# Kernel optimization log

Hardware: AMD Instinct MI355X
Metric: run time of the kernel (lower is better)

The kernel has to match this reference:

```python
import jax, jax.numpy as jnp
import numpy as np

DIM, HID, BATCH = 64, 512, 8192


def setup_inputs() -> dict:
    key = jax.random.key(0)
    ks = jax.random.split(key, 6)
    s1 = 1.0 / np.sqrt(DIM + 1)
    s2 = 1.0 / np.sqrt(HID)
    return {
        "t": jax.random.uniform(ks[0], (1,), dtype=jnp.float32),
        "x": jax.random.normal(ks[1], (BATCH, DIM), dtype=jnp.float32),
        "W1": jax.random.normal(ks[2], (DIM + 1, HID), dtype=jnp.float32) * s1,
        "b1": jnp.zeros((HID,), jnp.float32),
        "W2": jax.random.normal(ks[3], (HID, HID), dtype=jnp.float32) * s2,
        "b2": jnp.zeros((HID,), jnp.float32),
        "W3": jax.random.normal(ks[4], (HID, DIM), dtype=jnp.float32) * s2,
        "b3": jnp.zeros((DIM,), jnp.float32),
    }


def _vf_single(ts, xs, W1, b1, W2, b2, W3, b3):
    # xs: [dim], ts: scalar. Time concatenated as extra input feature.
    h = jnp.concatenate([xs, ts[None]])          # [dim+1]
    h = jnp.tanh(h @ W1 + b1)                    # [hid]
    h = jnp.tanh(h @ W2 + b2)                    # [hid]
    return h @ W3 + b3                           # [dim]


def reference(t, x, W1, b1, W2, b2, W3, b3):
    ts = t[0]
    vf = lambda xs: _vf_single(ts, xs, W1, b1, W2, b2, W3, b3)
    v = jax.vmap(vf)(x)                                   # [B, dim]
    # Exact divergence: trace of per-sample Jacobian dv/dx.
    # (Replaces the torch per-dim autograd.grad loop with one batched jacfwd.)
    J = jax.vmap(jax.jacfwd(vf))(x)                       # [B, dim, dim]
    div = jnp.trace(J, axis1=-2, axis2=-1)                # [B]
    return (v, -div[:, None])
```

## Files before the change

### kernel.cpp

```cpp
#include <hip/hip_runtime.h>

#define DIM 64
#define HID 512
#define BATCH 8192
#define MB 32
#define NTHR 1024

typedef __attribute__((ext_vector_type(8))) short short8;
typedef __attribute__((ext_vector_type(4))) float f32x4;
typedef __attribute__((ext_vector_type(16))) float f32x16;
typedef float float4_ __attribute__((ext_vector_type(4)));
typedef unsigned long long ull;

#define Z16 {0.f,0.f,0.f,0.f,0.f,0.f,0.f,0.f,0.f,0.f,0.f,0.f,0.f,0.f,0.f,0.f}

union U8 { short8 s8; unsigned short u[8]; };
union U4 { ull v; unsigned short u[4]; };
union FB { unsigned u; float f; };

__device__ __forceinline__ unsigned short f2bf(float f) {
    union { float f; unsigned u; } v; v.f = f;
    return (unsigned short)((v.u + 0x7FFFu + ((v.u >> 16) & 1u)) >> 16);
}
__device__ __forceinline__ float bf2f(unsigned short b) {
    FB v; v.u = (unsigned)b << 16; return v.f;
}
__device__ __forceinline__ float tanh_fast(float x) {
    float e = __expf(2.f * x);
    return 1.f - __fdividef(2.f, e + 1.f);
}

__global__ __launch_bounds__(256) void prep(
        const float* __restrict__ t,  const float* __restrict__ W1,
        const float* __restrict__ b1, const float* __restrict__ W2,
        const float* __restrict__ W3,
        unsigned short* __restrict__ w2pk, unsigned short* __restrict__ ppk,
        unsigned short* __restrict__ w3pk, unsigned short* __restrict__ w1pk,
        float* __restrict__ c1) {
    __shared__ float w3sT[DIM * 33];
    __shared__ float w1s[DIM * DIM];
    int b = blockIdx.x;
    if (b >= 288) {
        int n = (b - 288) * 256 + threadIdx.x;
        c1[n] = fmaf(t[0], W1[DIM * HID + n], b1[n]);
        return;
    }
    int gid = b * 256 + threadIdx.x;
    int f = gid >> 6, l = gid & 63;
    if (f < 512) {
        int nt = f >> 5, ks = f & 31;
        int n = nt * 32 + (l & 31), k0 = ks * 16 + (l >> 5) * 8;
        unsigned short* o = w2pk + (size_t)(f * 64 + l) * 8;
#pragma unroll
        for (int e = 0; e < 8; ++e) o[e] = f2bf(W2[(size_t)(k0 + e) * HID + n]);
    } else if (f < 1024) {
        int ntb = (b * 4 - 512) >> 5;
        int jb  = (((b - 128) * 4) & 31) * 16;
        for (int idx = threadIdx.x; idx < 32 * DIM; idx += 256) {
            int dn = idx >> 6, i = idx & 63;
            w3sT[i * 33 + dn] = W3[(size_t)(ntb * 32 + dn) * DIM + i];
        }
        for (int idx = threadIdx.x; idx < DIM * DIM; idx += 256) {
            int i = idx >> 6, jj = idx & 63;
            w1s[i * DIM + jj] = W1[(size_t)i * HID + jb + jj];
        }
        __syncthreads();
        int fi = f - 512;
        int ks = fi & 31;
        int dn = l & 31, k0 = ks * 16 + (l >> 5) * 8;
        int n = ntb * 32 + dn;
        int jo = k0 - jb;
        float m[8] = {0.f,0.f,0.f,0.f,0.f,0.f,0.f,0.f};
#pragma unroll
        for (int i = 0; i < DIM; ++i) {
            float w3 = w3sT[i * 33 + dn];
            const float* wrow = &w1s[i * DIM + jo];
#pragma unroll
            for (int e = 0; e < 8; ++e) m[e] = fmaf(wrow[e], w3, m[e]);
        }
        unsigned short* o = ppk + (size_t)(fi * 64 + l) * 8;
#pragma unroll
        for (int e = 0; e < 8; ++e) o[e] = f2bf(W2[(size_t)(k0 + e) * HID + n] * m[e]);
    } else if (f < 1088) {
        int fi = f - 1024;
        int nt = fi >> 4, ks = fi & 15;
        int n = nt * 16 + (l & 15), k0 = ks * 32 + (l >> 4) * 8;
        unsigned short* o = w3pk + (size_t)(fi * 64 + l) * 8;
#pragma unroll
        for (int e = 0; e < 8; ++e) o[e] = f2bf(W3[(size_t)(k0 + e) * DIM + n]);
    } else {
        int fi = f - 1088;
        int nt = fi >> 1, ks = fi & 1;
        int n = nt * 16 + (l & 15), k0 = ks * 32 + (l >> 4) * 8;
        unsigned short* o = w1pk + (size_t)(fi * 64 + l) * 8;
#pragma unroll
        for (int e = 0; e < 8; ++e) o[e] = f2bf(W1[(size_t)(k0 + e) * HID + n]);
    }
}

__device__ __forceinline__ int act_addr(int sample, int colbyte) {
    return (sample * 1024 + colbyte) ^ ((sample & 15) << 4);
}

__global__ __launch_bounds__(NTHR)
__attribute__((amdgpu_waves_per_eu(4, 4)))
void fused_main(
        const float* __restrict__ x,  const float* __restrict__ c1,
        const float* __restrict__ b2, const float* __restrict__ b3,
        const unsigned short* __restrict__ w1pk, const unsigned short* __restrict__ w2pk,
        const unsigned short* __restrict__ ppk,  const unsigned short* __restrict__ w3pk,
        float* __restrict__ out) {
    __shared__ unsigned short h1s[MB * HID];
    __shared__ unsigned short d1s[MB * HID];
    __shared__ unsigned short h2s[MB * HID];
    __shared__ float wred[8][MB];
    char* h1b = (char*)h1s; char* d1b = (char*)d1s; char* h2b = (char*)h2s;

    const int tid = threadIdx.x, w = tid >> 6, l = tid & 63;
    const int lr = l & 15, g = l >> 4;
    const int bid = blockIdx.x;
    const int s0 = bid * MB;

    short8 xf[2][2];
#pragma unroll
    for (int nt = 0; nt < 2; ++nt)
#pragma unroll
        for (int ks = 0; ks < 2; ++ks) {
            const float* xp = x + (size_t)(s0 + nt * 16 + lr) * DIM + ks * 32 + g * 8;
            float4_ x0 = *(const float4_*)xp;
            float4_ x1 = *(const float4_*)(xp + 4);
            U8 u;
            u.u[0]=f2bf(x0.x); u.u[1]=f2bf(x0.y); u.u[2]=f2bf(x0.z); u.u[3]=f2bf(x0.w);
            u.u[4]=f2bf(x1.x); u.u[5]=f2bf(x1.y); u.u[6]=f2bf(x1.z); u.u[7]=f2bf(x1.w);
            xf[nt][ks] = u.s8;
        }
#pragma unroll
    for (int mi = 0; mi < 2; ++mi) {
        int mt = w * 2 + mi;
        short8 a0 = ((const short8*)w1pk)[(size_t)((mt * 2 + 0) * 64 + l)];
        short8 a1 = ((const short8*)w1pk)[(size_t)((mt * 2 + 1) * 64 + l)];
        float c1q[4];
#pragma unroll
        for (int r = 0; r < 4; ++r) c1q[r] = c1[mt * 16 + g * 4 + r];
#pragma unroll
        for (int nt = 0; nt < 2; ++nt) {
            f32x4 acc = {0.f, 0.f, 0.f, 0.f};
            acc = __builtin_amdgcn_mfma_f32_16x16x32_bf16(a0, xf[nt][0], acc, 0, 0, 0);
            acc = __builtin_amdgcn_mfma_f32_16x16x32_bf16(a1, xf[nt][1], acc, 0, 0, 0);
            int sample = nt * 16 + lr;
            U4 hu, du;
#pragma unroll
            for (int r = 0; r < 4; ++r) {
                float h = tanh_fast(acc[r] + c1q[r]);
                hu.u[r] = f2bf(h);
                du.u[r] = f2bf(fmaf(-h, h, 1.f));
            }
            int ab = act_addr(sample, (mt * 16 + g * 4) * 2);
            *(ull*)(h1b + ab) = hu.v;
            *(ull*)(d1b + ab) = du.v;
        }
    }
    __syncthreads();

    const int q = w & 7, role = w >> 3;
    const int q2 = (q + bid) & 7;
    const short8* Bf = (const short8*)(role ? ppk : w2pk);
    const char* Ab = role ? d1b : h1b;
    const short8* b0p = Bf + (size_t)((2 * q2 + 0) * 32) * 64 + l;
    const short8* b1p = Bf + (size_t)((2 * q2 + 1) * 32) * 64 + l;
    const int rot = (bid * 5) & 31;
    f32x16 a0 = Z16, a1 = Z16;
#pragma unroll 4
    for (int i = 0; i < 32; ++i) {
        int ks = (i + rot) & 31;
        int ab = act_addr(l & 31, ks * 32 + (l >> 5) * 16);
        short8 av  = *(const short8*)(Ab + ab);
        short8 b0v = b0p[ks * 64];
        short8 b1v = b1p[ks * 64];
        a0 = __builtin_amdgcn_mfma_f32_32x32x16_bf16(av, b0v, a0, 0, 0, 0);
        a1 = __builtin_amdgcn_mfma_f32_32x32x16_bf16(av, b1v, a1, 0, 0, 0);
    }

    if (role == 0) {
#pragma unroll
        for (int j = 0; j < 2; ++j) {
            int c = (2 * q2 + j) * 32 + (l & 31);
            float b2v = b2[c];
            f32x16 acc = j ? a1 : a0;
#pragma unroll
            for (int r = 0; r < 16; ++r) {
                int row = (r & 3) + 8 * (r >> 2) + 4 * (l >> 5);
                float h2 = tanh_fast(acc[r] + b2v);
                *(unsigned short*)(h2b + act_addr(row, c * 2)) = f2bf(h2);
            }
        }
    }
    __syncthreads();

    if (role == 1) {
        float divp[16];
#pragma unroll
        for (int r = 0; r < 16; ++r) divp[r] = 0.f;
#pragma unroll
        for (int j = 0; j < 2; ++j) {
            int c = (2 * q2 + j) * 32 + (l & 31);
            f32x16 acc = j ? a1 : a0;
#pragma unroll
            for (int r = 0; r < 16; ++r) {
                int row = (r & 3) + 8 * (r >> 2) + 4 * (l >> 5);
                float h2 = bf2f(*(const unsigned short*)(h2b + act_addr(row, c * 2)));
                divp[r] = fmaf(acc[r], fmaf(-h2, h2, 1.f), divp[r]);
            }
        }
#pragma unroll
        for (int off = 1; off < 32; off <<= 1) {
#pragma unroll
            for (int r = 0; r < 16; ++r) divp[r] += __shfl_xor(divp[r], off, 64);
        }
        if ((l & 31) == 0) {
#pragma unroll
            for (int r = 0; r < 16; ++r) {
                int row = (r & 3) + 8 * (r >> 2) + 4 * (l >> 5);
                wred[q2][row] = divp[r];
            }
        }
    } else {
        const int wm3 = w & 1, wn3 = w >> 1;
        const int rot3 = (bid * 3) & 15;
        f32x4 acc = {0.f, 0.f, 0.f, 0.f};
        const short8* W3f = (const short8*)w3pk + (size_t)(wn3 * 16) * 64 + l;
#pragma unroll
        for (int i = 0; i < 16; ++i) {
            int ks = (i + rot3) & 15;
            short8 ah = *(const short8*)(h2b + act_addr(wm3 * 16 + lr, ks * 64 + g * 16));
            acc = __builtin_amdgcn_mfma_f32_16x16x32_bf16(ah, W3f[ks * 64], acc, 0, 0, 0);
        }
        int c = wn3 * 16 + lr;
        float b3v = b3[c];
#pragma unroll
        for (int r = 0; r < 4; ++r)
            out[(size_t)(s0 + wm3 * 16 + g * 4 + r) * DIM + c] = acc[r] + b3v;
    }
    __syncthreads();
    if (tid < MB) {
        float d = 0.f;
#pragma unroll
        for (int ww = 0; ww < 8; ++ww) d += wred[ww][tid];
        out[(size_t)BATCH * DIM + s0 + tid] = -d;
    }
}

extern "C" void kernel_launch(void* const* d_in, const int* in_sizes, int n_in,
                              void* d_out, int out_size, void* d_ws, size_t ws_size,
                              hipStream_t stream) {
    const float* t  = (const float*)d_in[0];
    const float* x  = (const float*)d_in[1];
    const float* W1 = (const float*)d_in[2];
    const float* b1 = (const float*)d_in[3];
    const float* W2 = (const float*)d_in[4];
    const float* b2 = (const float*)d_in[5];
    const float* W3 = (const float*)d_in[6];
    const float* b3 = (const float*)d_in[7];
    float* out = (float*)d_out;

    char* ws = (char*)d_ws;
    unsigned short* w2pk = (unsigned short*)ws;
    unsigned short* ppk  = (unsigned short*)(ws + (512 << 10));
    unsigned short* w3pk = (unsigned short*)(ws + (1 << 20));
    unsigned short* w1pk = (unsigned short*)(ws + (1 << 20) + (64 << 10));
    float*          c1   = (float*)(ws + (1 << 20) + (128 << 10));

    prep<<<290, 256, 0, stream>>>(t, W1, b1, W2, W3, w2pk, ppk, w3pk, w1pk, c1);
    fused_main<<<BATCH / MB, NTHR, 0, stream>>>(x, c1, b2, b3, w1pk, w2pk, ppk, w3pk, out);
}
```

Baseline: 32.79 us.

## Split hidden dimension across block pairs with 64-sample tiles and reduction kernel

Each block now handles 64 samples but only half of the layer-2 output columns, so every W2/P fragment loaded from global memory feeds two MFMAs (one per 32-sample half), which doubles weight reuse per load. Layer-1 is recomputed in full by both blocks of a pair, and the h2 buffer now aliases the d1 shared array, with an extra barrier added before it is overwritten. The partial layer-3 outputs and partial divergences are written to workspace and summed by a new reduce kernel that also adds b3. The trade-offs are an extra kernel launch, partial-result traffic through global memory, and redundant layer-1 work.

```diff
diff --git a/kernel.cpp b/kernel.cpp
--- a/kernel.cpp
+++ b/kernel.cpp
@@ -3,7 +3,7 @@
 #define DIM 64
 #define HID 512
 #define BATCH 8192
-#define MB 32
+#define MB 64
 #define NTHR 1024
 
 typedef __attribute__((ext_vector_type(8))) short short8;
@@ -83,8 +83,8 @@
         for (int e = 0; e < 8; ++e) o[e] = f2bf(W2[(size_t)(k0 + e) * HID + n] * m[e]);
     } else if (f < 1088) {
         int fi = f - 1024;
-        int nt = fi >> 4, ks = fi & 15;
-        int n = nt * 16 + (l & 15), k0 = ks * 32 + (l >> 4) * 8;
+        int hf = fi >> 5, nt = (fi >> 3) & 3, ks = fi & 7;
+        int n = nt * 16 + (l & 15), k0 = hf * 256 + ks * 32 + (l >> 4) * 8;
         unsigned short* o = w3pk + (size_t)(fi * 64 + l) * 8;
 #pragma unroll
         for (int e = 0; e < 8; ++e) o[e] = f2bf(W3[(size_t)(k0 + e) * DIM + n]);
@@ -101,29 +101,32 @@
 __device__ __forceinline__ int act_addr(int sample, int colbyte) {
     return (sample * 1024 + colbyte) ^ ((sample & 15) << 4);
 }
+__device__ __forceinline__ int h2_addr(int sample, int colbyte) {
+    return (sample * 512 + colbyte) ^ ((sample & 15) << 4);
+}
 
 __global__ __launch_bounds__(NTHR)
 __attribute__((amdgpu_waves_per_eu(4, 4)))
 void fused_main(
         const float* __restrict__ x,  const float* __restrict__ c1,
-        const float* __restrict__ b2, const float* __restrict__ b3,
+        const float* __restrict__ b2,
         const unsigned short* __restrict__ w1pk, const unsigned short* __restrict__ w2pk,
         const unsigned short* __restrict__ ppk,  const unsigned short* __restrict__ w3pk,
-        float* __restrict__ out) {
+        float* __restrict__ wsv, float* __restrict__ wsdiv) {
     __shared__ unsigned short h1s[MB * HID];
     __shared__ unsigned short d1s[MB * HID];
-    __shared__ unsigned short h2s[MB * HID];
     __shared__ float wred[8][MB];
-    char* h1b = (char*)h1s; char* d1b = (char*)d1s; char* h2b = (char*)h2s;
+    char* h1b = (char*)h1s; char* d1b = (char*)d1s; char* h2b = (char*)d1s;
 
     const int tid = threadIdx.x, w = tid >> 6, l = tid & 63;
     const int lr = l & 15, g = l >> 4;
     const int bid = blockIdx.x;
-    const int s0 = bid * MB;
-
-    short8 xf[2][2];
-#pragma unroll
-    for (int nt = 0; nt < 2; ++nt)
+    const int mtile = bid >> 1, half = bid & 1;
+    const int s0 = mtile * MB;
+
+    short8 xf[4][2];
+#pragma unroll
+    for (int nt = 0; nt < 4; ++nt)
 #pragma unroll
         for (int ks = 0; ks < 2; ++ks) {
             const float* xp = x + (size_t)(s0 + nt * 16 + lr) * DIM + ks * 32 + g * 8;
@@ -143,7 +146,7 @@
 #pragma unroll
         for (int r = 0; r < 4; ++r) c1q[r] = c1[mt * 16 + g * 4 + r];
 #pragma unroll
-        for (int nt = 0; nt < 2; ++nt) {
+        for (int nt = 0; nt < 4; ++nt) {
             f32x4 acc = {0.f, 0.f, 0.f, 0.f};
             acc = __builtin_amdgcn_mfma_f32_16x16x32_bf16(a0, xf[nt][0], acc, 0, 0, 0);
             acc = __builtin_amdgcn_mfma_f32_16x16x32_bf16(a1, xf[nt][1], acc, 0, 0, 0);
@@ -163,90 +166,102 @@
     __syncthreads();
 
     const int q = w & 7, role = w >> 3;
-    const int q2 = (q + bid) & 7;
-    const short8* Bf = (const short8*)(role ? ppk : w2pk);
+    const int ntg = half * 8 + q;
+    const short8* Bs = (const short8*)(role ? ppk : w2pk) + (size_t)(ntg * 32) * 64 + l;
     const char* Ab = role ? d1b : h1b;
-    const short8* b0p = Bf + (size_t)((2 * q2 + 0) * 32) * 64 + l;
-    const short8* b1p = Bf + (size_t)((2 * q2 + 1) * 32) * 64 + l;
     const int rot = (bid * 5) & 31;
-    f32x16 a0 = Z16, a1 = Z16;
+    f32x16 aA = Z16, aB = Z16;
 #pragma unroll 4
     for (int i = 0; i < 32; ++i) {
         int ks = (i + rot) & 31;
-        int ab = act_addr(l & 31, ks * 32 + (l >> 5) * 16);
-        short8 av  = *(const short8*)(Ab + ab);
-        short8 b0v = b0p[ks * 64];
-        short8 b1v = b1p[ks * 64];
-        a0 = __builtin_amdgcn_mfma_f32_32x32x16_bf16(av, b0v, a0, 0, 0, 0);
-        a1 = __builtin_amdgcn_mfma_f32_32x32x16_bf16(av, b1v, a1, 0, 0, 0);
-    }
+        int cb = ks * 32 + (l >> 5) * 16;
+        short8 bv = Bs[ks * 64];
+        short8 fA = *(const short8*)(Ab + act_addr(l & 31, cb));
+        short8 fB = *(const short8*)(Ab + act_addr(32 + (l & 31), cb));
+        aA = __builtin_amdgcn_mfma_f32_32x32x16_bf16(fA, bv, aA, 0, 0, 0);
+        aB = __builtin_amdgcn_mfma_f32_32x32x16_bf16(fB, bv, aB, 0, 0, 0);
+    }
+    __syncthreads();
 
     if (role == 0) {
+        int lc = q * 32 + (l & 31);
+        float b2v = b2[half * 256 + lc];
 #pragma unroll
         for (int j = 0; j < 2; ++j) {
-            int c = (2 * q2 + j) * 32 + (l & 31);
-            float b2v = b2[c];
-            f32x16 acc = j ? a1 : a0;
+            f32x16 acc = j ? aB : aA;
 #pragma unroll
             for (int r = 0; r < 16; ++r) {
-                int row = (r & 3) + 8 * (r >> 2) + 4 * (l >> 5);
-                float h2 = tanh_fast(acc[r] + b2v);
-                *(unsigned short*)(h2b + act_addr(row, c * 2)) = f2bf(h2);
+                int sample = j * 32 + (r & 3) + 8 * (r >> 2) + 4 * (l >> 5);
+                *(unsigned short*)(h2b + h2_addr(sample, lc * 2)) =
+                    f2bf(tanh_fast(acc[r] + b2v));
             }
         }
     }
     __syncthreads();
 
     if (role == 1) {
-        float divp[16];
-#pragma unroll
-        for (int r = 0; r < 16; ++r) divp[r] = 0.f;
+        int lc = q * 32 + (l & 31);
 #pragma unroll
         for (int j = 0; j < 2; ++j) {
-            int c = (2 * q2 + j) * 32 + (l & 31);
-            f32x16 acc = j ? a1 : a0;
+            f32x16 acc = j ? aB : aA;
+            float dp[16];
 #pragma unroll
             for (int r = 0; r < 16; ++r) {
-                int row = (r & 3) + 8 * (r >> 2) + 4 * (l >> 5);
-                float h2 = bf2f(*(const unsigned short*)(h2b + act_addr(row, c * 2)));
-                divp[r] = fmaf(acc[r], fmaf(-h2, h2, 1.f), divp[r]);
-            }
-        }
-#pragma unroll
-        for (int off = 1; off < 32; off <<= 1) {
-#pragma unroll
-            for (int r = 0; r < 16; ++r) divp[r] += __shfl_xor(divp[r], off, 64);
-        }
-        if ((l & 31) == 0) {
-#pragma unroll
-            for (int r = 0; r < 16; ++r) {
-                int row = (r & 3) + 8 * (r >> 2) + 4 * (l >> 5);
-                wred[q2][row] = divp[r];
+                int rm = (r & 3) + 8 * (r >> 2) + 4 * (l >> 5);
+                float h2 = bf2f(*(const unsigned short*)(h2b + h2_addr(j * 32 + rm, lc * 2)));
+                dp[r] = acc[r] * fmaf(-h2, h2, 1.f);
+            }
+#pragma unroll
+            for (int off = 1; off < 32; off <<= 1) {
+#pragma unroll
+                for (int r = 0; r < 16; ++r) dp[r] += __shfl_xor(dp[r], off, 64);
+            }
+            if ((l & 31) == 0) {
+#pragma unroll
+                for (int r = 0; r < 16; ++r) {
+                    int rm = (r & 3) + 8 * (r >> 2) + 4 * (l >> 5);
+                    wred[q][j * 32 + rm] = dp[r];
+                }
             }
         }
     } else {
-        const int wm3 = w & 1, wn3 = w >> 1;
-        const int rot3 = (bid * 3) & 15;
-        f32x4 acc = {0.f, 0.f, 0.f, 0.f};
-        const short8* W3f = (const short8*)w3pk + (size_t)(wn3 * 16) * 64 + l;
-#pragma unroll
-        for (int i = 0; i < 16; ++i) {
-            int ks = (i + rot3) & 15;
-            short8 ah = *(const short8*)(h2b + act_addr(wm3 * 16 + lr, ks * 64 + g * 16));
-            acc = __builtin_amdgcn_mfma_f32_16x16x32_bf16(ah, W3f[ks * 64], acc, 0, 0, 0);
-        }
-        int c = wn3 * 16 + lr;
-        float b3v = b3[c];
-#pragma unroll
-        for (int r = 0; r < 4; ++r)
-            out[(size_t)(s0 + wm3 * 16 + g * 4 + r) * DIM + c] = acc[r] + b3v;
+#pragma unroll
+        for (int jj = 0; jj < 2; ++jj) {
+            int p = q * 2 + jj, mt = p >> 2, ntv = p & 3;
+            f32x4 acc3 = {0.f, 0.f, 0.f, 0.f};
+            const short8* W3f = (const short8*)w3pk + (size_t)((half * 32 + ntv * 8) * 64) + l;
+#pragma unroll
+            for (int ks = 0; ks < 8; ++ks) {
+                short8 ah = *(const short8*)(h2b + h2_addr(mt * 16 + lr, ks * 64 + g * 16));
+                acc3 = __builtin_amdgcn_mfma_f32_16x16x32_bf16(ah, W3f[ks * 64], acc3, 0, 0, 0);
+            }
+#pragma unroll
+            for (int r = 0; r < 4; ++r)
+                wsv[(size_t)bid * 4096 + (mt * 16 + g * 4 + r) * 64 + ntv * 16 + lr] = acc3[r];
+        }
     }
     __syncthreads();
     if (tid < MB) {
         float d = 0.f;
 #pragma unroll
         for (int ww = 0; ww < 8; ++ww) d += wred[ww][tid];
-        out[(size_t)BATCH * DIM + s0 + tid] = -d;
+        wsdiv[bid * 64 + tid] = d;
+    }
+}
+
+__global__ __launch_bounds__(1024) void reduce_k(
+        const float* __restrict__ wsv, const float* __restrict__ wsdiv,
+        const float* __restrict__ b3, float* __restrict__ out) {
+    int idx = blockIdx.x * 1024 + threadIdx.x;
+    int sample = idx >> 6, dcol = idx & 63;
+    int m = sample >> 6, sl = sample & 63;
+    float v = wsv[(size_t)(2 * m) * 4096 + sl * 64 + dcol]
+            + wsv[(size_t)(2 * m + 1) * 4096 + sl * 64 + dcol] + b3[dcol];
+    out[idx] = v;
+    if (idx < BATCH) {
+        int m2 = idx >> 6, sl2 = idx & 63;
+        out[(size_t)BATCH * DIM + idx] =
+            -(wsdiv[(2 * m2) * 64 + sl2] + wsdiv[(2 * m2 + 1) * 64 + sl2]);
     }
 }
 
@@ -269,7 +284,10 @@
     unsigned short* w3pk = (unsigned short*)(ws + (1 << 20));
     unsigned short* w1pk = (unsigned short*)(ws + (1 << 20) + (64 << 10));
     float*          c1   = (float*)(ws + (1 << 20) + (128 << 10));
-
-    prep<<<290, 256, 0, stream>>>(t, W1, b1, W2, W3, w2pk, ppk, w3pk, w1pk, c1);
-    fused_main<<<BATCH / MB, NTHR, 0, stream>>>(x, c1, b2, b3, w1pk, w2pk, ppk, w3pk, out);
-}
+    float*          wsv  = (float*)(ws + (1 << 20) + (192 << 10));
+    float*          wsdiv= (float*)(ws + (1 << 20) + (192 << 10) + (4 << 20));
+
+    prep      <<<290, 256, 0, stream>>>(t, W1, b1, W2, W3, w2pk, ppk, w3pk, w1pk, c1);
+    fused_main<<<(BATCH / MB) * 2, NTHR, 0, stream>>>(x, c1, b2, w1pk, w2pk, ppk, w3pk, wsv, wsdiv);
+    reduce_k  <<<(BATCH * DIM) / 1024, 1024, 0, stream>>>(wsv, wsdiv, b3, out);
+}
```

Measured after the change: 41.70 us. 1.27x slower.
